# Kernel optimization log

Hardware: AMD Instinct MI355X
Metric: run time of the kernel (lower is better)

The kernel has to match this reference:

```python
import jax, jax.numpy as jnp
import numpy as np

B, N_IN, F_IN = 256, 128, 64   # x: (B, input_format[0], input_format[1])
G, F_OUT = 128, 64             # output_format
S = 16                         # sparse_num


def setup_inputs() -> dict:
    key = jax.random.key(0)
    k1, k2, k3, k4 = jax.random.split(key, 4)
    x = jax.random.normal(k1, (B, N_IN, F_IN), dtype=jnp.float32)
    idx = jax.random.randint(k2, (G, S), 0, N_IN)                  # pair_params stacked
    fan_in = F_IN * S
    bound_w = (6.0 / fan_in) ** 0.5  # kaiming_uniform a=sqrt(5) -> U(-sqrt(6/fan_in)*.. ); approx scale
    W = jax.random.uniform(k3, (G, F_OUT, F_IN * S), dtype=jnp.float32,
                           minval=-bound_w, maxval=bound_w)
    bound_b = 1.0 / (fan_in ** 0.5)
    b = jax.random.uniform(k4, (G, F_OUT), dtype=jnp.float32,
                           minval=-bound_b, maxval=bound_b)
    return {"x": x, "idx": idx, "W": W, "b": b}


def reference(x, idx, W, b):
    # Per-group gather over dim 1, flatten, linear, stack -> (B, G, F_OUT).
    g = x[:, idx, :]                         # (B, G, S, F_IN) fancy-index gather
    g = g.reshape(B, G, S * F_IN)            # (B, G, S*F_IN)
    out = jnp.einsum('bgk,gok->bgo', g, W) + b[None, :, :]  # (B, G, F_OUT)
    return out
```

## Files before the change

kernel.cpp:

```cpp
#include <hip/hip_runtime.h>
#include <hip/hip_bf16.h>

#define B_SZ   256
#define N_IN   128
#define F_IN   64
#define G_SZ   128
#define F_OUT  64
#define S_SZ   16
#define K_TOT  1024

#define M_TILE 128
#define BK     64
#define NSTEP  16
#define THREADS 512

#define LDSTRIDE 72

typedef __attribute__((ext_vector_type(8))) short short8;
typedef __attribute__((ext_vector_type(4))) float f32x4;
typedef unsigned short u16;
typedef unsigned int   u32;

static __device__ __forceinline__ u32 packbf2(float a, float b) {
    __hip_bfloat162 h = __float22bfloat162_rn(make_float2(a, b));
    union { __hip_bfloat162 h; u32 u; } c; c.h = h;
    return c.u;
}

__global__ __launch_bounds__(THREADS)
void sparse_linear_kernel(const float* __restrict__ x,
                          const int*   __restrict__ idx,
                          const float* __restrict__ W,
                          const float* __restrict__ bias,
                          float*       __restrict__ out)
{
    __shared__ u16 Alds[2][M_TILE * LDSTRIDE];
    __shared__ u16 Wlds[2][F_OUT * LDSTRIDE];

    const int blk   = blockIdx.x;
    const int g     = blk & 127;
    const int mt    = blk >> 7;
    const int bbase = mt * M_TILE;

    const int tid  = threadIdx.x;
    const int wave = tid >> 6;
    const int lane = tid & 63;
    const int wr   = wave >> 1;
    const int wc   = wave & 1;
    const int lmod = lane & 15;
    const int ldiv = lane >> 4;

    const float* aptr[4]; int lofsA[4];
    #pragma unroll
    for (int i = 0; i < 4; ++i) {
        int id = tid + i * THREADS;
        int m  = id >> 4;
        int f  = (id & 15) << 2;
        aptr[i]  = x + (size_t)(bbase + m) * (N_IN * F_IN) + f;
        lofsA[i] = m * (LDSTRIDE * 2) + f * 2;
    }
    const float* wptr[2]; int lofsW[2];
    #pragma unroll
    for (int i = 0; i < 2; ++i) {
        int id = tid + i * THREADS;
        int o  = id >> 4;
        int f  = (id & 15) << 2;
        wptr[i]  = W + (size_t)g * (F_OUT * K_TOT) + (size_t)o * K_TOT + f;
        lofsW[i] = o * (LDSTRIDE * 2) + f * 2;
    }

    int rows[NSTEP];
    #pragma unroll
    for (int s = 0; s < NSTEP; ++s) rows[s] = idx[g * S_SZ + s];

    f32x4  acc[2][2] = {};
    float4 ra[3][4], rw[3][2];

    #define LOADT(t, s)                                                        \
        {                                                                      \
            const int row = rows[t];                                           \
            _Pragma("unroll")                                                  \
            for (int i = 0; i < 4; ++i)                                        \
                ra[s][i] = *reinterpret_cast<const float4*>(aptr[i] + row * F_IN); \
            _Pragma("unroll")                                                  \
            for (int i = 0; i < 2; ++i)                                        \
                rw[s][i] = *reinterpret_cast<const float4*>(wptr[i] + (t) * BK);   \
        }

    #define STORET(s, buf)                                                     \
        {                                                                      \
            _Pragma("unroll")                                                  \
            for (int i = 0; i < 4; ++i) {                                      \
                uint2 p;                                                       \
                p.x = packbf2(ra[s][i].x, ra[s][i].y);                         \
                p.y = packbf2(ra[s][i].z, ra[s][i].w);                         \
                *reinterpret_cast<uint2*>(                                     \
                    reinterpret_cast<char*>(Alds[buf]) + lofsA[i]) = p;        \
            }                                                                  \
            _Pragma("unroll")                                                  \
            for (int i = 0; i < 2; ++i) {                                      \
                uint2 p;                                                       \
                p.x = packbf2(rw[s][i].x, rw[s][i].y);                         \
                p.y = packbf2(rw[s][i].z, rw[s][i].w);                         \
                *reinterpret_cast<uint2*>(                                     \
                    reinterpret_cast<char*>(Wlds[buf]) + lofsW[i]) = p;        \
            }                                                                  \
        }

    #define COMPUTE(buf)                                                       \
        {                                                                      \
            _Pragma("unroll")                                                  \
            for (int ks = 0; ks < 2; ++ks) {                                   \
                const int kb = ks * 32 + (ldiv << 3);                          \
                short8 a[2], bfr[2];                                           \
                _Pragma("unroll")                                              \
                for (int mi = 0; mi < 2; ++mi)                                 \
                    a[mi] = *reinterpret_cast<const short8*>(                  \
                        reinterpret_cast<const char*>(Alds[buf]) +             \
                        (wr * 32 + mi * 16 + lmod) * (LDSTRIDE * 2) + kb * 2); \
                _Pragma("unroll")                                              \
                for (int ni = 0; ni < 2; ++ni)                                 \
                    bfr[ni] = *reinterpret_cast<const short8*>(                \
                        reinterpret_cast<const char*>(Wlds[buf]) +             \
                        (wc * 32 + ni * 16 + lmod) * (LDSTRIDE * 2) + kb * 2); \
                _Pragma("unroll")                                              \
                for (int mi = 0; mi < 2; ++mi)                                 \
                    _Pragma("unroll")                                          \
                    for (int ni = 0; ni < 2; ++ni)                             \
                        acc[mi][ni] = __builtin_amdgcn_mfma_f32_16x16x32_bf16( \
                            a[mi], bfr[ni], acc[mi][ni], 0, 0, 0);             \
            }                                                                  \
        }

    #define ROLL_BARRIER()                                                     \
        {                                                                      \
            asm volatile("s_waitcnt lgkmcnt(0)" ::: "memory");                 \
            __builtin_amdgcn_s_barrier();                                      \
            asm volatile("" ::: "memory");                                     \
        }

    LOADT(0, 0);
    LOADT(1, 1);
    LOADT(2, 2);
    STORET(0, 0);
    ROLL_BARRIER();

    #pragma unroll
    for (int t = 0; t < NSTEP; ++t) {
        if (t + 3 < NSTEP) LOADT(t + 3, t % 3);
        COMPUTE(t & 1);
        if (t + 1 < NSTEP) {
            STORET((t + 1) % 3, (t + 1) & 1);
            ROLL_BARRIER();
        }
    }

    const int rowbase = bbase + wr * 32 + (ldiv << 2);
    #pragma unroll
    for (int ni = 0; ni < 2; ++ni) {
        const int o  = wc * 32 + ni * 16 + lmod;
        const float bv = bias[g * F_OUT + o];
        #pragma unroll
        for (int mi = 0; mi < 2; ++mi) {
            #pragma unroll
            for (int r = 0; r < 4; ++r) {
                const int brow = rowbase + mi * 16 + r;
                out[(size_t)brow * (G_SZ * F_OUT) + g * F_OUT + o] = acc[mi][ni][r] + bv;
            }
        }
    }
}

extern "C" void kernel_launch(void* const* d_in, const int* in_sizes, int n_in,
                              void* d_out, int out_size, void* d_ws, size_t ws_size,
                              hipStream_t stream) {
    const float* x    = (const float*)d_in[0];
    const int*   idx  = (const int*)d_in[1];
    const float* W    = (const float*)d_in[2];
    const float* bias = (const float*)d_in[3];
    float*       out  = (float*)d_out;

    sparse_linear_kernel<<<dim3(G_SZ * (B_SZ / M_TILE)), dim3(THREADS), 0, stream>>>(
        x, idx, W, bias, out);
}
```

Measured before the change: 23.66 us.

## Pre-convert x to bf16 and stream gathered rows directly to LDS

Adds a pre-pass kernel that converts all of x to bf16 in the workspace. The main kernel then gathers A tiles with global_load_lds into a triple-buffered, XOR-swizzled LDS layout, instead of loading fp32 into registers, converting and storing. The intent is to halve gather traffic, free registers and drop conversion work from the main loop. In exchange it adds a second launch that converts all 8 MB of x, plus a naive fallback path for when the workspace is too small.

New measurement: 25.68 us. 8.6% more time.

```diff
diff --git a/kernel.cpp b/kernel.cpp
--- a/kernel.cpp
+++ b/kernel.cpp
@@ -14,28 +14,41 @@
 #define NSTEP  16
 #define THREADS 512
 
-#define LDSTRIDE 72
+#define WSTRIDE 72
 
 typedef __attribute__((ext_vector_type(8))) short short8;
 typedef __attribute__((ext_vector_type(4))) float f32x4;
 typedef unsigned short u16;
 typedef unsigned int   u32;
 
+#define XN (B_SZ * N_IN * F_IN)
+
 static __device__ __forceinline__ u32 packbf2(float a, float b) {
     __hip_bfloat162 h = __float22bfloat162_rn(make_float2(a, b));
     union { __hip_bfloat162 h; u32 u; } c; c.h = h;
     return c.u;
 }
 
+__global__ __launch_bounds__(256)
+void convert_x_kernel(const float* __restrict__ x, u16* __restrict__ xbf) {
+    const int i = blockIdx.x * 256 + threadIdx.x;
+    const float4 v0 = reinterpret_cast<const float4*>(x)[i * 2];
+    const float4 v1 = reinterpret_cast<const float4*>(x)[i * 2 + 1];
+    uint4 p;
+    p.x = packbf2(v0.x, v0.y); p.y = packbf2(v0.z, v0.w);
+    p.z = packbf2(v1.x, v1.y); p.w = packbf2(v1.z, v1.w);
+    reinterpret_cast<uint4*>(xbf)[i] = p;
+}
+
 __global__ __launch_bounds__(THREADS)
-void sparse_linear_kernel(const float* __restrict__ x,
+void sparse_linear_kernel(const u16*   __restrict__ xbf,
                           const int*   __restrict__ idx,
                           const float* __restrict__ W,
                           const float* __restrict__ bias,
                           float*       __restrict__ out)
 {
-    __shared__ u16 Alds[2][M_TILE * LDSTRIDE];
-    __shared__ u16 Wlds[2][F_OUT * LDSTRIDE];
+    __shared__ u16 Alds[3][M_TILE * 64];
+    __shared__ u16 Wlds[2][F_OUT * WSTRIDE];
 
     const int blk   = blockIdx.x;
     const int g     = blk & 127;
@@ -50,15 +63,17 @@
     const int lmod = lane & 15;
     const int ldiv = lane >> 4;
 
-    const float* aptr[4]; int lofsA[4];
-    #pragma unroll
-    for (int i = 0; i < 4; ++i) {
-        int id = tid + i * THREADS;
-        int m  = id >> 4;
-        int f  = (id & 15) << 2;
-        aptr[i]  = x + (size_t)(bbase + m) * (N_IN * F_IN) + f;
-        lofsA[i] = m * (LDSTRIDE * 2) + f * 2;
-    }
+    const u16* arow[2]; int adst[2];
+    #pragma unroll
+    for (int i = 0; i < 2; ++i) {
+        int id   = tid + i * THREADS;
+        int m    = id >> 3;
+        int slot = id & 7;
+        arow[i] = xbf + ((size_t)(bbase + m) << 13)
+                      + (((slot * 16) ^ ((m & 7) << 4)) >> 1);
+        adst[i] = id * 8;
+    }
+
     const float* wptr[2]; int lofsW[2];
     #pragma unroll
     for (int i = 0; i < 2; ++i) {
@@ -66,7 +81,7 @@
         int o  = id >> 4;
         int f  = (id & 15) << 2;
         wptr[i]  = W + (size_t)g * (F_OUT * K_TOT) + (size_t)o * K_TOT + f;
-        lofsW[i] = o * (LDSTRIDE * 2) + f * 2;
+        lofsW[i] = o * (WSTRIDE * 2) + f * 2;
     }
 
     int rows[NSTEP];
@@ -74,29 +89,31 @@
     for (int s = 0; s < NSTEP; ++s) rows[s] = idx[g * S_SZ + s];
 
     f32x4  acc[2][2] = {};
-    float4 ra[3][4], rw[3][2];
-
-    #define LOADT(t, s)                                                        \
-        {                                                                      \
-            const int row = rows[t];                                           \
-            _Pragma("unroll")                                                  \
-            for (int i = 0; i < 4; ++i)                                        \
-                ra[s][i] = *reinterpret_cast<const float4*>(aptr[i] + row * F_IN); \
+    float4 rw[2][2];
+
+    #define STAGEA(t, buf)                                                     \
+        {                                                                      \
+            _Pragma("unroll")                                                  \
+            for (int i = 0; i < 2; ++i) {                                      \
+                const u16* gp = arow[i] + (rows[t] << 6);                      \
+                __builtin_amdgcn_global_load_lds(                              \
+                    (const __attribute__((address_space(1))) void*)gp,         \
+                    (__attribute__((address_space(3))) void*)                  \
+                        (&Alds[buf][adst[i]]),                                 \
+                    16, 0, 0);                                                 \
+            }                                                                  \
+            asm volatile("" ::: "memory");                                     \
+        }
+
+    #define LOADW(t, s)                                                        \
+        {                                                                      \
             _Pragma("unroll")                                                  \
             for (int i = 0; i < 2; ++i)                                        \
-                rw[s][i] = *reinterpret_cast<const float4*>(wptr[i] + (t) * BK);   \
-        }
-
-    #define STORET(s, buf)                                                     \
-        {                                                                      \
-            _Pragma("unroll")                                                  \
-            for (int i = 0; i < 4; ++i) {                                      \
-                uint2 p;                                                       \
-                p.x = packbf2(ra[s][i].x, ra[s][i].y);                         \
-                p.y = packbf2(ra[s][i].z, ra[s][i].w);                         \
-                *reinterpret_cast<uint2*>(                                     \
-                    reinterpret_cast<char*>(Alds[buf]) + lofsA[i]) = p;        \
-            }                                                                  \
+                rw[s][i] = *reinterpret_cast<const float4*>(wptr[i] + (t) * BK); \
+        }
+
+    #define STOREW(s, buf)                                                     \
+        {                                                                      \
             _Pragma("unroll")                                                  \
             for (int i = 0; i < 2; ++i) {                                      \
                 uint2 p;                                                       \
@@ -107,22 +124,24 @@
             }                                                                  \
         }
 
-    #define COMPUTE(buf)                                                       \
+    #define COMPUTE(abuf, wbuf)                                                \
         {                                                                      \
             _Pragma("unroll")                                                  \
             for (int ks = 0; ks < 2; ++ks) {                                   \
-                const int kb = ks * 32 + (ldiv << 3);                          \
+                const int kb2 = ks * 64 + ldiv * 16;        \
                 short8 a[2], bfr[2];                                           \
                 _Pragma("unroll")                                              \
-                for (int mi = 0; mi < 2; ++mi)                                 \
+                for (int mi = 0; mi < 2; ++mi) {                               \
+                    const int r = wr * 32 + mi * 16 + lmod;                    \
                     a[mi] = *reinterpret_cast<const short8*>(                  \
-                        reinterpret_cast<const char*>(Alds[buf]) +             \
-                        (wr * 32 + mi * 16 + lmod) * (LDSTRIDE * 2) + kb * 2); \
+                        reinterpret_cast<const char*>(Alds[abuf]) +            \
+                        r * 128 + (kb2 ^ ((r & 7) << 4)));                     \
+                }                                                              \
                 _Pragma("unroll")                                              \
                 for (int ni = 0; ni < 2; ++ni)                                 \
                     bfr[ni] = *reinterpret_cast<const short8*>(                \
-                        reinterpret_cast<const char*>(Wlds[buf]) +             \
-                        (wc * 32 + ni * 16 + lmod) * (LDSTRIDE * 2) + kb * 2); \
+                        reinterpret_cast<const char*>(Wlds[wbuf]) +            \
+                        (wc * 32 + ni * 16 + lmod) * (WSTRIDE * 2) + kb2);     \
                 _Pragma("unroll")                                              \
                 for (int mi = 0; mi < 2; ++mi)                                 \
                     _Pragma("unroll")                                          \
@@ -134,23 +153,27 @@
 
     #define ROLL_BARRIER()                                                     \
         {                                                                      \
-            asm volatile("s_waitcnt lgkmcnt(0)" ::: "memory");                 \
+            asm volatile("s_waitcnt vmcnt(4) lgkmcnt(0)" ::: "memory");        \
             __builtin_amdgcn_s_barrier();                                      \
             asm volatile("" ::: "memory");                                     \
         }
 
-    LOADT(0, 0);
-    LOADT(1, 1);
-    LOADT(2, 2);
-    STORET(0, 0);
+    STAGEA(0, 0);
+    STAGEA(1, 1);
+    LOADW(0, 0);
+    LOADW(1, 1);
+    STOREW(0, 0);
     ROLL_BARRIER();
 
     #pragma unroll
     for (int t = 0; t < NSTEP; ++t) {
-        if (t + 3 < NSTEP) LOADT(t + 3, t % 3);
-        COMPUTE(t & 1);
+        if (t + 2 < NSTEP) {
+            STAGEA(t + 2, (t + 2) % 3);
+            LOADW(t + 2, t & 1);
+        }
+        COMPUTE(t % 3, t & 1);
         if (t + 1 < NSTEP) {
-            STORET((t + 1) % 3, (t + 1) & 1);
+            STOREW((t + 1) & 1, (t + 1) & 1);
             ROLL_BARRIER();
         }
     }
@@ -171,6 +194,23 @@
     }
 }
 
+__global__ __launch_bounds__(256)
+void naive_kernel(const float* __restrict__ x, const int* __restrict__ idx,
+                  const float* __restrict__ W, const float* __restrict__ bias,
+                  float* __restrict__ out) {
+    const int i = blockIdx.x * 256 + threadIdx.x;
+    const int o = i & 63, gg = (i >> 6) & 127, b = i >> 13;
+    float s = bias[gg * F_OUT + o];
+    for (int t = 0; t < S_SZ; ++t) {
+        const int r = idx[gg * S_SZ + t];
+        #pragma unroll 8
+        for (int f = 0; f < F_IN; ++f)
+            s += x[(size_t)b * (N_IN * F_IN) + r * F_IN + f]
+               * W[(size_t)gg * (F_OUT * K_TOT) + (size_t)o * K_TOT + t * F_IN + f];
+    }
+    out[i] = s;
+}
+
 extern "C" void kernel_launch(void* const* d_in, const int* in_sizes, int n_in,
                               void* d_out, int out_size, void* d_ws, size_t ws_size,
                               hipStream_t stream) {
@@ -180,6 +220,14 @@
     const float* bias = (const float*)d_in[3];
     float*       out  = (float*)d_out;
 
-    sparse_linear_kernel<<<dim3(G_SZ * (B_SZ / M_TILE)), dim3(THREADS), 0, stream>>>(
-        x, idx, W, bias, out);
-}
+    const size_t need = (size_t)XN * sizeof(u16);
+    if (ws_size >= need) {
+        u16* xbf = (u16*)d_ws;
+        convert_x_kernel<<<dim3(XN / 8 / 256), dim3(256), 0, stream>>>(x, xbf);
+        sparse_linear_kernel<<<dim3(G_SZ * (B_SZ / M_TILE)), dim3(THREADS), 0, stream>>>(
+            xbf, idx, W, bias, out);
+    } else {
+        naive_kernel<<<dim3((B_SZ * G_SZ * F_OUT) / 256), dim3(256), 0, stream>>>(
+            x, idx, W, bias, out);
+    }
+}
```

## Split K across two blocks with atomic accumulation into zeroed output

Applied to the files above, without the earlier changes.

Splits the K dimension (16 sparse slots) in half so each group/M-tile pair is handled by two blocks, doubling the grid from 256 to 512 blocks to better fill the GPU's compute units. Output is zeroed with a memset and the partial sums are combined via float atomicAdd, with bias added only by the first half. The prefetch depth drops from three to two stages and launch bounds request four blocks per CU. The cost is an extra memset, atomic traffic on the 8 MB output, and non-deterministic summation order.

New measurement: 37.28 us. 57.6% more time.

```diff
diff --git a/kernel.cpp b/kernel.cpp
--- a/kernel.cpp
+++ b/kernel.cpp
@@ -11,7 +11,7 @@
 
 #define M_TILE 128
 #define BK     64
-#define NSTEP  16
+#define NHALF  8
 #define THREADS 512
 
 #define LDSTRIDE 72
@@ -27,7 +27,7 @@
     return c.u;
 }
 
-__global__ __launch_bounds__(THREADS)
+__global__ __launch_bounds__(THREADS, 4)
 void sparse_linear_kernel(const float* __restrict__ x,
                           const int*   __restrict__ idx,
                           const float* __restrict__ W,
@@ -39,7 +39,9 @@
 
     const int blk   = blockIdx.x;
     const int g     = blk & 127;
-    const int mt    = blk >> 7;
+    const int rest  = blk >> 7;
+    const int mt    = rest & 1;
+    const int kh    = rest >> 1;
     const int bbase = mt * M_TILE;
 
     const int tid  = threadIdx.x;
@@ -65,16 +67,18 @@
         int id = tid + i * THREADS;
         int o  = id >> 4;
         int f  = (id & 15) << 2;
-        wptr[i]  = W + (size_t)g * (F_OUT * K_TOT) + (size_t)o * K_TOT + f;
+        wptr[i]  = W + (size_t)g * (F_OUT * K_TOT) + (size_t)o * K_TOT
+                     + kh * (NHALF * BK) + f;
         lofsW[i] = o * (LDSTRIDE * 2) + f * 2;
     }
 
-    int rows[NSTEP];
+    int rows[NHALF];
     #pragma unroll
-    for (int s = 0; s < NSTEP; ++s) rows[s] = idx[g * S_SZ + s];
+    for (int s = 0; s < NHALF; ++s)
+        rows[s] = idx[g * S_SZ + kh * NHALF + s];
 
     f32x4  acc[2][2] = {};
-    float4 ra[3][4], rw[3][2];
+    float4 ra[2][4], rw[2][2];
 
     #define LOADT(t, s)                                                        \
         {                                                                      \
@@ -141,16 +145,15 @@
 
     LOADT(0, 0);
     LOADT(1, 1);
-    LOADT(2, 2);
     STORET(0, 0);
     ROLL_BARRIER();
 
     #pragma unroll
-    for (int t = 0; t < NSTEP; ++t) {
-        if (t + 3 < NSTEP) LOADT(t + 3, t % 3);
+    for (int t = 0; t < NHALF; ++t) {
+        if (t + 2 < NHALF) LOADT(t + 2, t & 1);
         COMPUTE(t & 1);
-        if (t + 1 < NSTEP) {
-            STORET((t + 1) % 3, (t + 1) & 1);
+        if (t + 1 < NHALF) {
+            STORET((t + 1) & 1, (t + 1) & 1);
             ROLL_BARRIER();
         }
     }
@@ -159,13 +162,14 @@
     #pragma unroll
     for (int ni = 0; ni < 2; ++ni) {
         const int o  = wc * 32 + ni * 16 + lmod;
-        const float bv = bias[g * F_OUT + o];
+        const float bv = (kh == 0) ? bias[g * F_OUT + o] : 0.0f;
         #pragma unroll
         for (int mi = 0; mi < 2; ++mi) {
             #pragma unroll
             for (int r = 0; r < 4; ++r) {
                 const int brow = rowbase + mi * 16 + r;
-                out[(size_t)brow * (G_SZ * F_OUT) + g * F_OUT + o] = acc[mi][ni][r] + bv;
+                atomicAdd(&out[(size_t)brow * (G_SZ * F_OUT) + g * F_OUT + o],
+                          acc[mi][ni][r] + bv);
             }
         }
     }
@@ -180,6 +184,8 @@
     const float* bias = (const float*)d_in[3];
     float*       out  = (float*)d_out;
 
-    sparse_linear_kernel<<<dim3(G_SZ * (B_SZ / M_TILE)), dim3(THREADS), 0, stream>>>(
+    hipMemsetAsync(out, 0, (size_t)out_size * sizeof(float), stream);
+
+    sparse_linear_kernel<<<dim3(512), dim3(THREADS), 0, stream>>>(
         x, idx, W, bias, out);
 }
```
